# Kernel tuning notes

Hardware: AMD Instinct MI355X
Metric: run time of the kernel (lower is better)

## Reference

```python
import jax, jax.numpy as jnp
import numpy as np

EPS = 1e-09
TOP_K = 2


def setup_inputs() -> dict:
    key = jax.random.key(0)
    ks = jax.random.split(key, 6)
    B, L, F, E, D, SE = 64, 1024, 900, 8, 768, 64
    cycle_curve_data = jax.random.normal(ks[0], (B, L, F), dtype=jnp.float32)
    logits = jax.random.normal(ks[1], (B, E), dtype=jnp.float32)
    moe_masks = jax.random.randint(ks[2], (B, E), 0, 2, dtype=jnp.int32)
    selection_embeddings = jax.random.normal(ks[3], (B, E, SE), dtype=jnp.float32)
    W = jax.random.normal(ks[4], (E, F, D), dtype=jnp.float32) * 0.02
    b = jnp.zeros((E, D), dtype=jnp.float32)
    return {"cycle_curve_data": cycle_curve_data, "logits": logits,
            "moe_masks": moe_masks, "selection_embeddings": selection_embeddings,
            "W": W, "b": b}


def reference(cycle_curve_data, logits, moe_masks, selection_embeddings, W, b):
    B = cycle_curve_data.shape[0]
    E = logits.shape[1]
    mask = (moe_masks == 1).astype(logits.dtype)                 # [B, E]
    raw = jax.nn.softmax(logits, axis=1)                         # [B, E]
    p = raw * mask
    # selection embedding from inactive experts
    inactive = raw * (1.0 - mask)
    inactive = inactive / (jnp.sum(inactive, axis=1, keepdims=True) + EPS)
    selection_embedding = jnp.sum(selection_embeddings * inactive[:, :, None], axis=1)  # [B, SE]
    # top-k masking (indices treated as constants, same as torch scatter mask)
    if TOP_K > 0:
        _, idx = jax.lax.top_k(p, TOP_K)                         # [B, K]
        topk_mask = jnp.zeros_like(p).at[jnp.arange(B)[:, None], idx].set(1.0)
        p = p * topk_mask
    p = p / (jnp.sum(p, axis=1, keepdims=True) + EPS)            # [B, E]
    # dispatch/combine == weighted sum of per-expert Linear outputs
    # (weights are zero for unselected experts, matching MOEDispatcher)
    out = jnp.zeros(cycle_curve_data.shape[:2] + (W.shape[-1],), dtype=cycle_curve_data.dtype)
    for e in range(E):  # small fixed expert count
        expert_out = jnp.einsum('blf,fd->bld', cycle_curve_data, W[e]) + b[e]
        out = out + p[:, e, None, None] * expert_out
    final_out = out.astype(jnp.bfloat16)
    # guide loss (training mode)
    s = jnp.sum(raw * mask) / B
    guide_loss = (1.0 - s) * (1.0 - s)
    return final_out, guide_loss, selection_embedding
```

## Files before the change

kernel.cpp:

```cpp
#include <hip/hip_runtime.h>

#define B_  64
#define L_  1024
#define F_  900
#define E_  8
#define D_  768
#define SE_ 64
#define KP_ 928
#define FD_ (F_*D_)
#define OUT_MAIN (64*1024*768)
#define GL_OFF   OUT_MAIN
#define SE_OFF   (OUT_MAIN + 1)
#define EPSF 1e-9f
#define NT_  29


using f32x4  = __attribute__((ext_vector_type(4))) float;
using bf16   = __bf16;
using bf16x4 = __attribute__((ext_vector_type(4))) __bf16;
using bf16x8 = __attribute__((ext_vector_type(8))) __bf16;
using s16x8  = __attribute__((ext_vector_type(8))) short;

__device__ __forceinline__ f32x4 mfma_bf16(bf16x8 a, bf16x8 b, f32x4 c) {
  return __builtin_amdgcn_mfma_f32_16x16x32_bf16(
      __builtin_bit_cast(s16x8, a), __builtin_bit_cast(s16x8, b), c, 0, 0, 0);
}

__device__ __forceinline__ void gload16(const bf16* g, bf16* l) {
  __builtin_amdgcn_global_load_lds(
      (const __attribute__((address_space(1))) unsigned int*)g,
      (__attribute__((address_space(3))) unsigned int*)l, 16, 0, 0);
}

__device__ __forceinline__ const unsigned* pick_masks(const void* cA, const void* cB,
                                                      const float** logits) {
  const unsigned* a = (const unsigned*)cA;
  bool aIsMask = true;
#pragma unroll
  for (int i = 0; i < 512; i += 37) aIsMask &= (a[i] <= 1u);
  if (aIsMask) { *logits = (const float*)cB; return a; }
  *logits = (const float*)cA; return (const unsigned*)cB;
}

struct Gate { int e1, e2; float p1, p2; };

__device__ __forceinline__ Gate gate_for(const float* __restrict__ logits,
                                         const unsigned* __restrict__ masks, int b) {
  float lg[E_]; unsigned mk[E_];
#pragma unroll
  for (int e = 0; e < E_; ++e) { lg[e] = logits[b*E_+e]; mk[e] = masks[b*E_+e]; }
  float mx = lg[0];
#pragma unroll
  for (int e = 1; e < E_; ++e) mx = fmaxf(mx, lg[e]);
  float ex[E_], s = 0.f;
#pragma unroll
  for (int e = 0; e < E_; ++e) { ex[e] = expf(lg[e]-mx); s += ex[e]; }
  const float inv_s = 1.f / s;
  float p0[E_];
#pragma unroll
  for (int e = 0; e < E_; ++e) p0[e] = (mk[e] == 1u) ? ex[e]*inv_s : 0.f;
  int e1 = 0;
#pragma unroll
  for (int e = 1; e < E_; ++e) if (p0[e] > p0[e1]) e1 = e;
  int e2 = (e1 == 0) ? 1 : 0;
#pragma unroll
  for (int e = 0; e < E_; ++e) if (e != e1 && p0[e] > p0[e2]) e2 = e;
  const float inv = 1.f / (p0[e1] + p0[e2] + EPSF);
  Gate g; g.e1 = e1; g.e2 = e2; g.p1 = p0[e1]*inv; g.p2 = p0[e2]*inv;
  return g;
}

__global__ void gating_kernel(const void* cA, const void* cB,
                              const float* __restrict__ selemb,
                              float* __restrict__ fout) {
  const float* logits; const unsigned* masks = pick_masks(cA, cB, &logits);
  const int b = threadIdx.x;
  float lg[E_]; unsigned mk[E_];
#pragma unroll
  for (int e = 0; e < E_; ++e) { lg[e] = logits[b*E_+e]; mk[e] = masks[b*E_+e]; }
  float mx = lg[0];
#pragma unroll
  for (int e = 1; e < E_; ++e) mx = fmaxf(mx, lg[e]);
  float ex[E_], s = 0.f;
#pragma unroll
  for (int e = 0; e < E_; ++e) { ex[e] = expf(lg[e]-mx); s += ex[e]; }
  const float inv_s = 1.f / s;
  float inact[E_]; float isum = 0.f, sact = 0.f;
#pragma unroll
  for (int e = 0; e < E_; ++e) {
    float raw = ex[e] * inv_s;
    if (mk[e] == 1u) { sact += raw; inact[e] = 0.f; }
    else             { inact[e] = raw; isum += raw; }
  }
  const float inv_i = 1.f / (isum + EPSF);
  for (int se = 0; se < SE_; ++se) {
    float a = 0.f;
#pragma unroll
    for (int e = 0; e < E_; ++e)
      a += inact[e] * inv_i * selemb[((size_t)b*E_ + e)*SE_ + se];
    fout[SE_OFF + b*SE_ + se] = a;
  }
#pragma unroll
  for (int off = 32; off > 0; off >>= 1) sact += __shfl_down(sact, off);
  if (b == 0) {
    float sm = sact / (float)B_;
    fout[GL_OFF] = (1.f - sm) * (1.f - sm);
  }
}

__global__ __launch_bounds__(256) void xconv_kernel(const float* __restrict__ X,
                                                    bf16* __restrict__ Xbf) {
  const size_t row = blockIdx.x;
  const int t = threadIdx.x;
  const float* src = X + row * F_;
  bf16* dst = Xbf + row * KP_;
  if (t < 225) {
    f32x4 v = *(const f32x4*)(src + t*4);
    bf16x4 o;
#pragma unroll
    for (int j = 0; j < 4; ++j) o[j] = (bf16)v[j];
    *(bf16x4*)(dst + t*4) = o;
  } else if (t < 232) {
    bf16x4 z = (bf16x4){(bf16)0.f,(bf16)0.f,(bf16)0.f,(bf16)0.f};
    *(bf16x4*)(dst + 900 + (t-225)*4) = z;
  }
}

__global__ __launch_bounds__(256) void wmix_kernel(const float* __restrict__ W,
                                                   const void* cA, const void* cB,
                                                   bf16* __restrict__ Wmix) {
  __shared__ float tile[32][33];
  const int b  = blockIdx.z;
  const int d0 = blockIdx.x << 5;
  const int f0 = blockIdx.y << 5;
  const float* logits; const unsigned* masks = pick_masks(cA, cB, &logits);
  const Gate g = gate_for(logits, masks, b);
  const float* W1 = W + (size_t)g.e1*FD_;
  const float* W2 = W + (size_t)g.e2*FD_;
  const int c = threadIdx.x & 31, r = threadIdx.x >> 5;
#pragma unroll
  for (int p = 0; p < 4; ++p) {
    int f = f0 + p*8 + r;
    float v = 0.f;
    if (f < F_) {
      size_t o = (size_t)f*D_ + d0 + c;
      v = g.p1*W1[o] + g.p2*W2[o];
    }
    tile[p*8+r][c] = v;
  }
  __syncthreads();
#pragma unroll
  for (int p = 0; p < 4; ++p) {
    int d = d0 + p*8 + r;
    Wmix[((size_t)b*D_ + d)*KP_ + f0 + c] = (bf16)tile[c][p*8+r];
  }
}

__global__ __launch_bounds__(256) void gemm_fast(
    const bf16* __restrict__ Xbf, const bf16* __restrict__ Wmix,
    const float* __restrict__ bias,
    const void* cA, const void* cB,
    float* __restrict__ fout) {
  __shared__ bf16 As[2][128*32];
  __shared__ bf16 Bs[2][128*32];

  const int id  = blockIdx.x;
  const int xcd = id & 7, q = id >> 3;
  const int b   = xcd + ((q / 48) << 3);
  const int j   = q % 48;
  const int bn  = j % 6, bm = j / 6;

  const float* logits; const unsigned* masks = pick_masks(cA, cB, &logits);
  const Gate g = gate_for(logits, masks, b);

  const bf16* Ab = Xbf  + ((size_t)b*L_ + (size_t)bm*128) * KP_;
  const bf16* Bb = Wmix + ((size_t)b*D_ + (size_t)bn*128) * KP_;

  const int t = threadIdx.x, lane = t & 63, w = t >> 6;
  const int sw   = ((lane & 3) ^ ((lane >> 2) & 3)) << 3;
  const int row0 = (w << 5) + (lane >> 2);
  const int row1 = row0 + 16;
  const int dst0 = (w << 7) << 3;
  const int dst1 = dst0 + (64 << 3);

  auto STAGE = [&](int buf, int kt) {
    const int k0 = kt << 5;
    gload16(Ab + (size_t)row0*KP_ + k0 + sw, &As[buf][dst0]);
    gload16(Ab + (size_t)row1*KP_ + k0 + sw, &As[buf][dst1]);
    gload16(Bb + (size_t)row0*KP_ + k0 + sw, &Bs[buf][dst0]);
    gload16(Bb + (size_t)row1*KP_ + k0 + sw, &Bs[buf][dst1]);
  };

  const int wr = (w >> 1) << 6, wc = (w & 1) << 6;
  const int fr = lane & 15, fks = lane >> 4;
  const int rq = (lane >> 4) << 2;

  int aoff[4], boff[4];
#pragma unroll
  for (int m = 0; m < 4; ++m) {
    int rA = wr + m*16 + fr;
    aoff[m] = rA*32 + ((fks ^ (rA & 3)) << 3);
    int rB = wc + m*16 + fr;
    boff[m] = rB*32 + ((fks ^ (rB & 3)) << 3);
  }

  f32x4 acc[4][4];
#pragma unroll
  for (int m = 0; m < 4; ++m)
#pragma unroll
    for (int n = 0; n < 4; ++n) acc[m][n] = (f32x4){0.f,0.f,0.f,0.f};

  STAGE(0, 0);
  int cur = 0;
  for (int kt = 0; kt < NT_; ++kt) {
    __syncthreads();
    if (kt + 1 < NT_) STAGE(cur ^ 1, kt + 1);
    bf16x8 af[4], bfv[4];
#pragma unroll
    for (int m = 0; m < 4; ++m) af[m]  = *(const bf16x8*)&As[cur][aoff[m]];
#pragma unroll
    for (int n = 0; n < 4; ++n) bfv[n] = *(const bf16x8*)&Bs[cur][boff[n]];
#pragma unroll
    for (int m = 0; m < 4; ++m)
#pragma unroll
      for (int n = 0; n < 4; ++n)
        acc[m][n] = mfma_bf16(af[m], bfv[n], acc[m][n]);
    cur ^= 1;
  }

  const float* b1 = bias + g.e1*D_;
  const float* b2 = bias + g.e2*D_;
#pragma unroll
  for (int n = 0; n < 4; ++n) {
    int gc = bn*128 + wc + n*16 + fr;
    float bs = g.p1*b1[gc] + g.p2*b2[gc];
#pragma unroll
    for (int m = 0; m < 4; ++m) {
      size_t base = ((size_t)b*L_ + (size_t)(bm*128 + wr + m*16 + rq)) * D_ + gc;
#pragma unroll
      for (int i = 0; i < 4; ++i)
        fout[base + (size_t)i*D_] = acc[m][n][i] + bs;
    }
  }
}

__global__ void transw_kernel(const float* __restrict__ W, bf16* __restrict__ Wt) {
  __shared__ float tile[32][33];
  const int e  = blockIdx.z;
  const int d0 = blockIdx.x << 5;
  const int f0 = blockIdx.y << 5;
  const int c = threadIdx.x & 31, r = threadIdx.x >> 5;
#pragma unroll
  for (int p = 0; p < 4; ++p) {
    int f = f0 + p*8 + r;
    tile[p*8+r][c] = (f < F_) ? W[((size_t)e*F_ + f)*D_ + d0 + c] : 0.f;
  }
  __syncthreads();
#pragma unroll
  for (int p = 0; p < 4; ++p) {
    int d = d0 + p*8 + r;
    Wt[((size_t)e*D_ + d)*KP_ + f0 + c] = (bf16)tile[c][p*8+r];
  }
}

__global__ __launch_bounds__(256) void gemm_kernel(
    const float* __restrict__ X, const bf16* __restrict__ Wt,
    const float* __restrict__ bias,
    const void* cA, const void* cB,
    float* __restrict__ fout) {
  __shared__ bf16 As[128][40];
  __shared__ bf16 Bs[128][40];
  const int bn = blockIdx.x, bm = blockIdx.y, b = blockIdx.z;
  const float* logits; const unsigned* masks = pick_masks(cA, cB, &logits);
  const Gate g = gate_for(logits, masks, b);
  const float* Xb = X + ((size_t)b*L_ + (size_t)bm*128) * F_;
  const bf16* W1 = Wt + ((size_t)g.e1*D_ + (size_t)bn*128) * KP_;
  const bf16* W2 = Wt + ((size_t)g.e2*D_ + (size_t)bn*128) * KP_;
  const int t  = threadIdx.x;
  const int ar = t >> 3, ac = (t & 7) << 2;
  const int br = t >> 2, bc = (t & 3) << 3;
  const int lane = t & 63, wave = t >> 6;
  const int wr = (wave >> 1) << 6, wc = (wave & 1) << 6;
  const int fr = lane & 15, fk = (lane >> 4) << 3;
  const int rq = (lane >> 4) << 2;
  f32x4 acc[4][4];
#pragma unroll
  for (int m = 0; m < 4; ++m)
#pragma unroll
    for (int n = 0; n < 4; ++n) acc[m][n] = (f32x4){0.f,0.f,0.f,0.f};
  f32x4 ax[4]; bf16x8 wv1[2], wv2[2];
  auto LOAD = [&](int k0) {
    if (k0 <= F_ - 32) {
#pragma unroll
      for (int p = 0; p < 4; ++p)
        ax[p] = *(const f32x4*)(Xb + (size_t)(p*32 + ar)*F_ + k0 + ac);
    } else {
#pragma unroll
      for (int p = 0; p < 4; ++p)
#pragma unroll
        for (int j = 0; j < 4; ++j) {
          int k = k0 + ac + j;
          ax[p][j] = (k < F_) ? Xb[(size_t)(p*32 + ar)*F_ + k] : 0.f;
        }
    }
#pragma unroll
    for (int p = 0; p < 2; ++p) {
      wv1[p] = *(const bf16x8*)(W1 + (size_t)(p*64 + br)*KP_ + k0 + bc);
      wv2[p] = *(const bf16x8*)(W2 + (size_t)(p*64 + br)*KP_ + k0 + bc);
    }
  };
  auto STAGE = [&]() {
#pragma unroll
    for (int p = 0; p < 4; ++p) {
      bf16x4 v;
#pragma unroll
      for (int j = 0; j < 4; ++j) v[j] = (bf16)ax[p][j];
      *(bf16x4*)&As[p*32 + ar][ac] = v;
    }
#pragma unroll
    for (int p = 0; p < 2; ++p) {
      bf16x8 v;
#pragma unroll
      for (int j = 0; j < 8; ++j)
        v[j] = (bf16)(g.p1 * (float)wv1[p][j] + g.p2 * (float)wv2[p][j]);
      *(bf16x8*)&Bs[p*64 + br][bc] = v;
    }
  };
  LOAD(0);
  for (int kt = 0; kt < NT_; ++kt) {
    STAGE();
    __syncthreads();
    if (kt + 1 < NT_) LOAD((kt + 1) << 5);
    bf16x8 af[4], bfv[4];
#pragma unroll
    for (int m = 0; m < 4; ++m) af[m]  = *(const bf16x8*)&As[wr + m*16 + fr][fk];
#pragma unroll
    for (int n = 0; n < 4; ++n) bfv[n] = *(const bf16x8*)&Bs[wc + n*16 + fr][fk];
#pragma unroll
    for (int m = 0; m < 4; ++m)
#pragma unroll
      for (int n = 0; n < 4; ++n)
        acc[m][n] = mfma_bf16(af[m], bfv[n], acc[m][n]);
    __syncthreads();
  }
  const float* b1 = bias + g.e1*D_;
  const float* b2 = bias + g.e2*D_;
#pragma unroll
  for (int n = 0; n < 4; ++n) {
    int gc = bn*128 + wc + n*16 + fr;
    float bs = g.p1*b1[gc] + g.p2*b2[gc];
#pragma unroll
    for (int m = 0; m < 4; ++m) {
      size_t base = ((size_t)b*L_ + (size_t)(bm*128 + wr + m*16 + rq)) * D_ + gc;
#pragma unroll
      for (int i = 0; i < 4; ++i)
        fout[base + (size_t)i*D_] = acc[m][n][i] + bs;
    }
  }
}

__global__ __launch_bounds__(128) void fallback_kernel(
    const float* __restrict__ X, const float* __restrict__ W,
    const float* __restrict__ bias,
    const void* cA, const void* cB,
    float* __restrict__ fout) {
  __shared__ float xs[16 * F_];
  const int t  = threadIdx.x;
  const int d  = blockIdx.x * 128 + t;
  const int l0 = blockIdx.y * 16;
  const int b  = blockIdx.z;
  const float* logits; const unsigned* masks = pick_masks(cA, cB, &logits);
  const Gate g = gate_for(logits, masks, b);
  const float* xrow = X + ((size_t)b*L_ + l0) * F_;
  for (int i = t; i < 16 * F_; i += 128) xs[i] = xrow[i];
  __syncthreads();
  const float* w1 = W + (size_t)g.e1*FD_ + d;
  const float* w2 = W + (size_t)g.e2*FD_ + d;
  float acc[16];
#pragma unroll
  for (int j = 0; j < 16; ++j) acc[j] = 0.f;
  for (int k = 0; k < F_; k += 4) {
    float wb[4];
#pragma unroll
    for (int q = 0; q < 4; ++q)
      wb[q] = g.p1 * w1[(size_t)(k+q)*D_] + g.p2 * w2[(size_t)(k+q)*D_];
#pragma unroll
    for (int j = 0; j < 16; ++j) {
      f32x4 xv = *(const f32x4*)&xs[j*F_ + k];
#pragma unroll
      for (int q = 0; q < 4; ++q) acc[j] += xv[q] * wb[q];
    }
  }
  const float bs = g.p1*bias[g.e1*D_+d] + g.p2*bias[g.e2*D_+d];
#pragma unroll
  for (int j = 0; j < 16; ++j)
    fout[((size_t)b*L_ + (size_t)(l0 + j)) * D_ + d] = acc[j] + bs;
}

extern "C" void kernel_launch(void* const* d_in, const int* in_sizes, int n_in,
                              void* d_out, int out_size, void* d_ws, size_t ws_size,
                              hipStream_t stream) {
  const float *X = nullptr, *selemb = nullptr, *W = nullptr, *bias = nullptr;
  const void *cA = nullptr, *cB = nullptr;
  for (int i = 0; i < n_in; ++i) {
    switch (in_sizes[i]) {
      case 58982400: X      = (const float*)d_in[i]; break;
      case 32768:    selemb = (const float*)d_in[i]; break;
      case 5529600:  W      = (const float*)d_in[i]; break;
      case 6144:     bias   = (const float*)d_in[i]; break;
      case 512:      if (!cA) cA = d_in[i]; else cB = d_in[i]; break;
      default: break;
    }
  }
  if (!X)      X      = (const float*)d_in[0];
  if (!cA)     cA     = d_in[1];
  if (!cB)     cB     = d_in[2];
  if (!selemb) selemb = (const float*)d_in[3];
  if (!W)      W      = (const float*)d_in[4];
  if (!bias)   bias   = (const float*)d_in[5];
  float* fout = (float*)d_out;

  const size_t xbf_bytes  = (size_t)B_*L_*KP_*2;
  const size_t wmix_bytes = (size_t)B_*D_*KP_*2;
  const size_t need_fast  = xbf_bytes + wmix_bytes;
  const size_t need_mid   = (size_t)E_*D_*KP_*2;

  gating_kernel<<<1, 64, 0, stream>>>(cA, cB, selemb, fout);

  if (ws_size >= need_fast) {
    bf16* Xbf  = (bf16*)d_ws;
    bf16* Wmix = (bf16*)((char*)d_ws + xbf_bytes);
    xconv_kernel<<<B_*L_, 256, 0, stream>>>(X, Xbf);
    wmix_kernel<<<dim3(24, 29, 64), 256, 0, stream>>>(W, cA, cB, Wmix);
    gemm_fast<<<3072, 256, 0, stream>>>(Xbf, Wmix, bias, cA, cB, fout);
  } else if (ws_size >= need_mid) {
    bf16* Wt = (bf16*)d_ws;
    transw_kernel<<<dim3(24, 29, 8), 256, 0, stream>>>(W, Wt);
    gemm_kernel<<<dim3(6, 8, 64), 256, 0, stream>>>(X, Wt, bias, cA, cB, fout);
  } else {
    fallback_kernel<<<dim3(6, 64, 64), 128, 0, stream>>>(X, W, bias, cA, cB, fout);
  }
}
```

Before: 417.6 us.

## Restructure conversion kernels and add explicit waitcnt barriers in GEMM loop

The X conversion kernel now processes 32 rows per block in a flattened loop instead of one row per block, cutting launch count. The W mixing kernel drops the shared-memory transpose and has each lane gather 8 consecutive f values into one 16-byte bf16x8 store, with 512 blocks. The GEMM main loop replaces __syncthreads with manual s_waitcnt vmcnt and s_barrier plus scheduling barriers, adding a second barrier after the MFMAs. These aim to lower launch overhead and improve overlap, but the vmcnt(4) count assumes STAGE issues exactly four loads, and the strided wmix reads may coalesce less well.

```diff
diff --git a/kernel.cpp b/kernel.cpp
--- a/kernel.cpp
+++ b/kernel.cpp
@@ -110,49 +110,53 @@
 
 __global__ __launch_bounds__(256) void xconv_kernel(const float* __restrict__ X,
                                                     bf16* __restrict__ Xbf) {
-  const size_t row = blockIdx.x;
-  const int t = threadIdx.x;
-  const float* src = X + row * F_;
-  bf16* dst = Xbf + row * KP_;
-  if (t < 225) {
-    f32x4 v = *(const f32x4*)(src + t*4);
+  const int r0 = blockIdx.x << 5;
+  const int t  = threadIdx.x;
+#pragma unroll 1
+  for (int it = 0; it < 29; ++it) {
+    int idx = it*256 + t;
+    int row = idx / 232, s = idx - row*232;
+    size_t gr = (size_t)(r0 + row);
     bf16x4 o;
-#pragma unroll
-    for (int j = 0; j < 4; ++j) o[j] = (bf16)v[j];
-    *(bf16x4*)(dst + t*4) = o;
-  } else if (t < 232) {
-    bf16x4 z = (bf16x4){(bf16)0.f,(bf16)0.f,(bf16)0.f,(bf16)0.f};
-    *(bf16x4*)(dst + 900 + (t-225)*4) = z;
+    if (s < 225) {
+      f32x4 v = *(const f32x4*)(X + gr*F_ + s*4);
+#pragma unroll
+      for (int j = 0; j < 4; ++j) o[j] = (bf16)v[j];
+    } else {
+      o = (bf16x4){(bf16)0.f,(bf16)0.f,(bf16)0.f,(bf16)0.f};
+    }
+    *(bf16x4*)(Xbf + gr*KP_ + s*4) = o;
   }
 }
 
 __global__ __launch_bounds__(256) void wmix_kernel(const float* __restrict__ W,
                                                    const void* cA, const void* cB,
                                                    bf16* __restrict__ Wmix) {
-  __shared__ float tile[32][33];
-  const int b  = blockIdx.z;
-  const int d0 = blockIdx.x << 5;
-  const int f0 = blockIdx.y << 5;
+  const int b   = blockIdx.x >> 3;
+  const int sub = blockIdx.x & 7;
   const float* logits; const unsigned* masks = pick_masks(cA, cB, &logits);
   const Gate g = gate_for(logits, masks, b);
   const float* W1 = W + (size_t)g.e1*FD_;
   const float* W2 = W + (size_t)g.e2*FD_;
-  const int c = threadIdx.x & 31, r = threadIdx.x >> 5;
-#pragma unroll
-  for (int p = 0; p < 4; ++p) {
-    int f = f0 + p*8 + r;
-    float v = 0.f;
-    if (f < F_) {
-      size_t o = (size_t)f*D_ + d0 + c;
-      v = g.p1*W1[o] + g.p2*W2[o];
-    }
-    tile[p*8+r][c] = v;
-  }
-  __syncthreads();
-#pragma unroll
-  for (int p = 0; p < 4; ++p) {
-    int d = d0 + p*8 + r;
-    Wmix[((size_t)b*D_ + d)*KP_ + f0 + c] = (bf16)tile[c][p*8+r];
+  const int w = threadIdx.x >> 6, lane = threadIdx.x & 63;
+  const int wid = sub*4 + w;
+#pragma unroll 1
+  for (int task = wid; task < 1392; task += 32) {
+    const int dc  = task / 116, oct = task - dc*116;
+    const int d   = (dc << 6) + lane;
+    const int f0  = oct << 3;
+    bf16x8 pk;
+#pragma unroll
+    for (int j = 0; j < 8; ++j) {
+      int f = f0 + j;
+      float v = 0.f;
+      if (f < F_) {
+        size_t o = (size_t)f*D_ + d;
+        v = g.p1*W1[o] + g.p2*W2[o];
+      }
+      pk[j] = (bf16)v;
+    }
+    *(bf16x8*)(Wmix + ((size_t)b*D_ + d)*KP_ + f0) = pk;
   }
 }
 
@@ -212,9 +216,17 @@
 
   STAGE(0, 0);
   int cur = 0;
+#pragma unroll 1
   for (int kt = 0; kt < NT_; ++kt) {
-    __syncthreads();
-    if (kt + 1 < NT_) STAGE(cur ^ 1, kt + 1);
+    if (kt + 1 < NT_) {
+      STAGE(cur ^ 1, kt + 1);
+      asm volatile("s_waitcnt vmcnt(4)" ::: "memory");
+    } else {
+      asm volatile("s_waitcnt vmcnt(0)" ::: "memory");
+    }
+    __builtin_amdgcn_sched_barrier(0);
+    __builtin_amdgcn_s_barrier();
+    __builtin_amdgcn_sched_barrier(0);
     bf16x8 af[4], bfv[4];
 #pragma unroll
     for (int m = 0; m < 4; ++m) af[m]  = *(const bf16x8*)&As[cur][aoff[m]];
@@ -225,6 +237,8 @@
 #pragma unroll
       for (int n = 0; n < 4; ++n)
         acc[m][n] = mfma_bf16(af[m], bfv[n], acc[m][n]);
+    __builtin_amdgcn_sched_barrier(0);
+    __builtin_amdgcn_s_barrier();
     cur ^= 1;
   }
 
@@ -430,8 +444,8 @@
   if (ws_size >= need_fast) {
     bf16* Xbf  = (bf16*)d_ws;
     bf16* Wmix = (bf16*)((char*)d_ws + xbf_bytes);
-    xconv_kernel<<<B_*L_, 256, 0, stream>>>(X, Xbf);
-    wmix_kernel<<<dim3(24, 29, 64), 256, 0, stream>>>(W, cA, cB, Wmix);
+    xconv_kernel<<<2048, 256, 0, stream>>>(X, Xbf);
+    wmix_kernel<<<512, 256, 0, stream>>>(W, cA, cB, Wmix);
     gemm_fast<<<3072, 256, 0, stream>>>(Xbf, Wmix, bias, cA, cB, fout);
   } else if (ws_size >= need_mid) {
     bf16* Wt = (bf16*)d_ws;
```

New measurement: 452.1 us. 1.08x slower.
